# Optimization experiments

Measured on AMD Instinct MI355X. Metric: run time of the kernel, lower is better.

Reference implementation:

```python
import jax, jax.numpy as jnp
import numpy as np

EMB = 768
HEADS = 12
DK = EMB // HEADS
DFF = 3072
LN_EPS = 1e-5


def _layernorm(x, g, b):
    mu = jnp.mean(x, axis=-1, keepdims=True)
    var = jnp.mean(jnp.square(x - mu), axis=-1, keepdims=True)
    return (x - mu) * jax.lax.rsqrt(var + LN_EPS) * g + b


def setup_inputs() -> dict:
    key = jax.random.key(0)
    ks = jax.random.split(key, 16)
    B, S = 16, 577
    s = 0.02
    inp = {
        "x": jax.random.normal(ks[0], (B, S, EMB), jnp.float32),
        # attention projections, stored as [in, out] so y = x @ W + b
        "wq": jax.random.normal(ks[1], (EMB, EMB), jnp.float32) * s,
        "bq": jnp.zeros((EMB,), jnp.float32),
        "wk": jax.random.normal(ks[2], (EMB, EMB), jnp.float32) * s,
        "bk": jnp.zeros((EMB,), jnp.float32),
        "wv": jax.random.normal(ks[3], (EMB, EMB), jnp.float32) * s,
        "bv": jnp.zeros((EMB,), jnp.float32),
        "wo": jax.random.normal(ks[4], (EMB, EMB), jnp.float32) * s,
        "bo": jnp.zeros((EMB,), jnp.float32),
        # feed-forward
        "w1": jax.random.normal(ks[5], (EMB, DFF), jnp.float32) * s,
        "bf1": jnp.zeros((DFF,), jnp.float32),
        "w2": jax.random.normal(ks[6], (DFF, EMB), jnp.float32) * s,
        "bf2": jnp.zeros((EMB,), jnp.float32),
        # layer norms
        "ln1_g": jnp.ones((EMB,), jnp.float32),
        "ln1_b": jnp.zeros((EMB,), jnp.float32),
        "ln2_g": jnp.ones((EMB,), jnp.float32),
        "ln2_b": jnp.zeros((EMB,), jnp.float32),
    }
    return inp


def reference(x, wq, bq, wk, bk, wv, bv, wo, bo, w1, bf1, w2, bf2,
              ln1_g, ln1_b, ln2_g, ln2_b):
    B, S, _ = x.shape
    # --- pre-LN + multi-head attention ---
    residual = x
    h = _layernorm(x, ln1_g, ln1_b)
    q = (h @ wq + bq).reshape(B, S, HEADS, DK)
    k = (h @ wk + bk).reshape(B, S, HEADS, DK)
    v = (h @ wv + bv).reshape(B, S, HEADS, DK)
    # NOTE: source applies softmax to UNSCALED scores (no 1/sqrt(d_k)).
    scores = jnp.einsum("bqhd,bkhd->bhqk", q, k)
    attn = jax.nn.softmax(scores.astype(jnp.float32), axis=-1)
    ctx = jnp.einsum("bhqk,bkhd->bqhd", attn, v).reshape(B, S, EMB)
    h = ctx @ wo + bo
    x = h + residual  # dropout is identity (eval / drop_rate=0)
    # --- pre-LN + feed-forward ---
    residual = x
    h = _layernorm(x, ln2_g, ln2_b)
    h = jax.nn.gelu(h @ w1 + bf1, approximate=False)
    h = h @ w2 + bf2
    return h + residual
```

## Files before the change

kernel.cpp:

```cpp
#include <hip/hip_runtime.h>
#include <hip/hip_bf16.h>
#include <math.h>

#define EMB 768
#define HEADS 12
#define DKH 64
#define DFF 3072
#define NB 16
#define SEQ 577
#define MTOK (NB*SEQ)
#define BHN (NB*HEADS)
#define VLD 640

typedef __attribute__((ext_vector_type(8))) short short8;
typedef __attribute__((ext_vector_type(4))) float f32x4;

__device__ __forceinline__ unsigned short f2bf(float f) {
  __hip_bfloat16 h = __float2bfloat16(f);
  return *reinterpret_cast<unsigned short*>(&h);
}

__device__ __forceinline__ float gelu_f(float x) {
  float u = x * (1.5957691216f + 0.0713548162726f * x * x);
  return x / (1.0f + __expf(-u));
}

__device__ __forceinline__ void gld_lds16(const unsigned short* g, unsigned short* l) {
  __builtin_amdgcn_global_load_lds(
      (const __attribute__((address_space(1))) unsigned int*)(g),
      (__attribute__((address_space(3))) unsigned int*)(l), 16, 0, 0);
}

template<int N> __device__ __forceinline__ void waitcnt_vm() {
  if constexpr (N == 0) asm volatile("s_waitcnt vmcnt(0)" ::: "memory");
  else if constexpr (N == 1) asm volatile("s_waitcnt vmcnt(1)" ::: "memory");
  else if constexpr (N == 2) asm volatile("s_waitcnt vmcnt(2)" ::: "memory");
  else if constexpr (N == 3) asm volatile("s_waitcnt vmcnt(3)" ::: "memory");
  else if constexpr (N == 4) asm volatile("s_waitcnt vmcnt(4)" ::: "memory");
}

__global__ __launch_bounds__(256) void ln_kernel(
    const float* __restrict__ x, const float* __restrict__ g,
    const float* __restrict__ b, unsigned short* __restrict__ out) {
  int row = blockIdx.x;
  int tid = threadIdx.x;
  const float* xr = x + (long)row * EMB;
  float v0 = xr[tid], v1 = xr[tid + 256], v2 = xr[tid + 512];
  float s = v0 + v1 + v2;
  float sq = v0*v0 + v1*v1 + v2*v2;
  for (int off = 32; off; off >>= 1) {
    s  += __shfl_down(s,  off, 64);
    sq += __shfl_down(sq, off, 64);
  }
  __shared__ float sh[8];
  int wid = tid >> 6, lane = tid & 63;
  if (lane == 0) { sh[wid] = s; sh[4 + wid] = sq; }
  __syncthreads();
  s  = sh[0] + sh[1] + sh[2] + sh[3];
  sq = sh[4] + sh[5] + sh[6] + sh[7];
  float mu = s * (1.0f / EMB);
  float var = sq * (1.0f / EMB) - mu * mu;
  float rs = rsqrtf(var + 1e-5f);
  unsigned short* orow = out + (long)row * EMB;
  orow[tid]       = f2bf((v0 - mu) * rs * g[tid]       + b[tid]);
  orow[tid + 256] = f2bf((v1 - mu) * rs * g[tid + 256] + b[tid + 256]);
  orow[tid + 512] = f2bf((v2 - mu) * rs * g[tid + 512] + b[tid + 512]);
}

__global__ __launch_bounds__(256) void transpose_all(
    const float* __restrict__ wq, const float* __restrict__ wk,
    const float* __restrict__ wv, const float* __restrict__ wo,
    const float* __restrict__ w1, const float* __restrict__ w2,
    unsigned short* __restrict__ WqkvT, unsigned short* __restrict__ WoT,
    unsigned short* __restrict__ W1T, unsigned short* __restrict__ W2T) {
  __shared__ float t[32][33];
  const int z = blockIdx.z;
  const int bx = blockIdx.x, by = blockIdx.y;
  const float* src; unsigned short* dst; int R, C, r0, c0;
  if (z < 4) {
    if (bx >= 24) return;
    R = 768; C = 768; r0 = by*32; c0 = bx*32;
    src = (z == 0) ? wq : (z == 1) ? wk : (z == 2) ? wv : wo;
    dst = (z == 0) ? WqkvT : (z == 1) ? WqkvT + 768*768 : (z == 2) ? WqkvT + 2*768*768 : WoT;
  } else if (z == 4) {
    R = 768; C = 3072; r0 = by*32; c0 = bx*32; src = w1; dst = W1T;
  } else {
    R = 3072; C = 768; r0 = bx*32; c0 = by*32; src = w2; dst = W2T;
  }
  int tx = threadIdx.x & 31, ty = threadIdx.x >> 5;
#pragma unroll
  for (int l = 0; l < 4; l++)
    t[ty + l*8][tx] = src[(long)(r0 + ty + l*8) * C + c0 + tx];
  __syncthreads();
#pragma unroll
  for (int l = 0; l < 4; l++)
    dst[(long)(c0 + ty + l*8) * R + r0 + tx] = f2bf(t[tx][ty + l*8]);
}

__global__ void concat_bias(const float* __restrict__ a, const float* __restrict__ b,
                            const float* __restrict__ c, float* __restrict__ o) {
  int i = blockIdx.x * 256 + threadIdx.x;
  if (i < 768) o[i] = a[i];
  else if (i < 1536) o[i] = b[i - 768];
  else if (i < 2304) o[i] = c[i - 1536];
}

__global__ __launch_bounds__(256) void transpose_v(
    const unsigned short* __restrict__ qkv, unsigned short* __restrict__ vT) {
  __shared__ unsigned short t[32][33];
  int bhi = blockIdx.z;
  int b = bhi / HEADS, h = bhi % HEADS;
  int s0 = blockIdx.x * 32, d0 = blockIdx.y * 32;
  int tx = threadIdx.x & 31, ty = threadIdx.x >> 5;
  const unsigned short* base = qkv + ((long)b * SEQ) * (3*EMB) + 2*EMB + h*DKH;
#pragma unroll
  for (int l = 0; l < 4; l++) {
    int s = s0 + ty + l*8;
    t[ty + l*8][tx] = (s < SEQ) ? base[(long)s * (3*EMB) + d0 + tx] : (unsigned short)0;
  }
  __syncthreads();
  unsigned short* ob = vT + ((long)bhi * DKH) * VLD;
#pragma unroll
  for (int l = 0; l < 4; l++) {
    int d = d0 + ty + l*8;
    int s = s0 + tx;
    if (s < SEQ) ob[(long)d * VLD + s] = t[tx][ty + l*8];
  }
}

template<bool BIAS, bool RESID, bool GELU_, bool OF32, int BM, int BN>
__global__ __launch_bounds__(256) void gemm_pipe(
    const unsigned short* __restrict__ A,
    const unsigned short* __restrict__ Bt,
    const float* __restrict__ bias,
    const float* __restrict__ resid,
    float* __restrict__ outf,
    unsigned short* __restrict__ outb,
    int M, int N, int K, int lda, int ldb, int ldc,
    int CX, int CY) {
  constexpr int MT = BM / 32, NT = BN / 32;
  constexpr int MA = BM / 64, NA = BN / 64;
  constexpr int L = MA + NA;
  __shared__ unsigned short As[2][BM * 32];
  __shared__ unsigned short Bs[2][BN * 32];

  const int bid = blockIdx.x;
  const int xcd = bid & 7;
  const int sidx = bid >> 3;
  const int colt = sidx % CX;
  const int band = (sidx / CX) * 8 + xcd;
  if (band >= CY) return;
  const int m0 = band * BM, n0 = colt * BN;

  const int tid = threadIdx.x;
  const int wave = tid >> 6, lane = tid & 63;
  const int wm = (wave >> 1) * (BM / 2), wn = (wave & 1) * (BN / 2);
  const int lm = lane & 15, q = lane >> 4;
  const int qs = ((q ^ ((lm >> 1) & 3)) * 8);

  const int srow = tid >> 2;
  const int scol = (((tid & 3) ^ ((tid >> 3) & 3)) * 8);
  int gmA[MA];
#pragma unroll
  for (int t = 0; t < MA; t++) {
    gmA[t] = m0 + srow + t * 64;
    if (gmA[t] > M - 1) gmA[t] = M - 1;
  }
  int gnB[NA];
#pragma unroll
  for (int t = 0; t < NA; t++) gnB[t] = n0 + srow + t * 64;

  auto stage = [&](int kIter, int buf) {
    const int k0 = kIter << 5;
#pragma unroll
    for (int t = 0; t < MA; t++)
      gld_lds16(A + (long)gmA[t] * lda + k0 + scol, &As[buf][8*tid + t*2048]);
#pragma unroll
    for (int t = 0; t < NA; t++)
      gld_lds16(Bt + (long)gnB[t] * ldb + k0 + scol, &Bs[buf][8*tid + t*2048]);
  };

  f32x4 acc[MT][NT];
#pragma unroll
  for (int i = 0; i < MT; i++)
#pragma unroll
    for (int j = 0; j < NT; j++) acc[i][j] = (f32x4){0,0,0,0};

  const int iters = K >> 5;
  stage(0, 0);
  for (int k = 0; k < iters; k++) {
    const int cur = k & 1;
    if (k + 1 < iters) {
      stage(k + 1, cur ^ 1);
      waitcnt_vm<L>();
    } else {
      waitcnt_vm<0>();
    }
    asm volatile("s_barrier" ::: "memory");

    short8 af[MT], bf[NT];
#pragma unroll
    for (int i = 0; i < MT; i++) af[i] = *(const short8*)&As[cur][(wm + i*16 + lm) * 32 + qs];
#pragma unroll
    for (int j = 0; j < NT; j++) bf[j] = *(const short8*)&Bs[cur][(wn + j*16 + lm) * 32 + qs];
#pragma unroll
    for (int i = 0; i < MT; i++)
#pragma unroll
      for (int j = 0; j < NT; j++)
        acc[i][j] = __builtin_amdgcn_mfma_f32_16x16x32_bf16(af[i], bf[j], acc[i][j], 0, 0, 0);

    asm volatile("s_waitcnt lgkmcnt(0)" ::: "memory");
    asm volatile("s_barrier" ::: "memory");
  }

#pragma unroll
  for (int i = 0; i < MT; i++) {
#pragma unroll
    for (int j = 0; j < NT; j++) {
      int col = n0 + wn + j*16 + lm;
      float bv = BIAS ? bias[col] : 0.0f;
#pragma unroll
      for (int r = 0; r < 4; r++) {
        int row = m0 + wm + i*16 + q*4 + r;
        if (row >= M) continue;
        float v = acc[i][j][r] + bv;
        if (RESID) v += resid[(long)row * ldc + col];
        if (GELU_) v = gelu_f(v);
        long o = (long)row * ldc + col;
        if (OF32)   outf[o] = v;
        else        outb[o] = f2bf(v);
      }
    }
  }
}

#define QT 128
__global__ __launch_bounds__(256) void flash_attn2(
    const unsigned short* __restrict__ qkv,
    const unsigned short* __restrict__ vT,
    unsigned short* __restrict__ ctx) {
  __shared__ unsigned short Qs[QT * 64];
  __shared__ unsigned short Ks[64 * 64];
  __shared__ unsigned short Vs[64 * 64];
  __shared__ unsigned short Ps[QT * 64];

  const int q0 = blockIdx.x * QT;
  const int bh = blockIdx.y;
  const int b = bh / HEADS, h = bh % HEADS;
  const int tid = threadIdx.x;
  const int wave = tid >> 6, lane = tid & 63;
  const int lm = lane & 15, q = lane >> 4;
  const int xlm = (lm >> 1) & 3;

  const int sr = tid >> 3;
  const int gcol = ((tid & 7) ^ ((sr >> 1) & 3)) * 8;

#pragma unroll
  for (int it = 0; it < 4; it++) {
    int r = sr + it*32;
    int s = q0 + r; if (s > SEQ - 1) s = SEQ - 1;
    gld_lds16(qkv + ((long)(b*SEQ + s))*(3*EMB) + h*DKH + gcol, &Qs[8*tid + it*2048]);
  }
  waitcnt_vm<0>();
  __syncthreads();

  short8 qf[2][2];
#pragma unroll
  for (int rt = 0; rt < 2; rt++)
#pragma unroll
    for (int kk = 0; kk < 2; kk++)
      qf[rt][kk] = *(const short8*)&Qs[(wave*32 + rt*16 + lm)*64 + ((kk*4 + q) ^ xlm)*8];

  f32x4 oacc[2][4];
  float lsum[2][4];
#pragma unroll
  for (int rt = 0; rt < 2; rt++)
#pragma unroll
    for (int j = 0; j < 4; j++) oacc[rt][j] = (f32x4){0,0,0,0};
#pragma unroll
  for (int rt = 0; rt < 2; rt++)
#pragma unroll
    for (int r = 0; r < 4; r++) lsum[rt][r] = 0.f;

  for (int kt = 0; kt < 10; kt++) {
    __syncthreads();
#pragma unroll
    for (int it = 0; it < 2; it++) {
      int r = sr + it*32;
      int s = kt*64 + r; if (s > SEQ - 1) s = SEQ - 1;
      gld_lds16(qkv + ((long)(b*SEQ + s))*(3*EMB) + EMB + h*DKH + gcol, &Ks[8*tid + it*2048]);
      gld_lds16(vT + ((long)bh*DKH + r)*VLD + (long)kt*64 + gcol, &Vs[8*tid + it*2048]);
    }
    waitcnt_vm<0>();
    __syncthreads();

    f32x4 sacc[2][4];
#pragma unroll
    for (int t = 0; t < 4; t++) {
      short8 kf0 = *(const short8*)&Ks[(t*16 + lm)*64 + ((0 + q) ^ xlm)*8];
      short8 kf1 = *(const short8*)&Ks[(t*16 + lm)*64 + ((4 + q) ^ xlm)*8];
      bool dead = (kt*64 + t*16 + lm) >= SEQ;
#pragma unroll
      for (int rt = 0; rt < 2; rt++) {
        f32x4 s0 = __builtin_amdgcn_mfma_f32_16x16x32_bf16(qf[rt][0], kf0, (f32x4){0,0,0,0}, 0, 0, 0);
        s0 = __builtin_amdgcn_mfma_f32_16x16x32_bf16(qf[rt][1], kf1, s0, 0, 0, 0);
        sacc[rt][t] = dead ? (f32x4){-1e30f,-1e30f,-1e30f,-1e30f} : s0;
      }
    }

#pragma unroll
    for (int rt = 0; rt < 2; rt++)
#pragma unroll
      for (int t = 0; t < 4; t++)
#pragma unroll
        for (int r = 0; r < 4; r++) {
          float p = __expf(sacc[rt][t][r] - 8.0f);
          lsum[rt][r] += p;
          int row = wave*32 + rt*16 + q*4 + r;
          int g = (t*2 + (lm >> 3)) ^ ((q*2 + (r >> 1)) & 3);
          Ps[row*64 + g*8 + (lm & 7)] = f2bf(p);
        }

#pragma unroll
    for (int kk = 0; kk < 2; kk++) {
      short8 vf[4];
#pragma unroll
      for (int j = 0; j < 4; j++)
        vf[j] = *(const short8*)&Vs[(j*16 + lm)*64 + ((kk*4 + q) ^ xlm)*8];
#pragma unroll
      for (int rt = 0; rt < 2; rt++) {
        short8 pf = *(const short8*)&Ps[(wave*32 + rt*16 + lm)*64 + ((kk*4 + q) ^ xlm)*8];
#pragma unroll
        for (int j = 0; j < 4; j++)
          oacc[rt][j] = __builtin_amdgcn_mfma_f32_16x16x32_bf16(pf, vf[j], oacc[rt][j], 0, 0, 0);
      }
    }
  }

#pragma unroll
  for (int rt = 0; rt < 2; rt++)
#pragma unroll
    for (int r = 0; r < 4; r++) {
      float l = lsum[rt][r];
      l += __shfl_xor(l, 1, 64);
      l += __shfl_xor(l, 2, 64);
      l += __shfl_xor(l, 4, 64);
      l += __shfl_xor(l, 8, 64);
      lsum[rt][r] = 1.0f / l;
    }

#pragma unroll
  for (int rt = 0; rt < 2; rt++)
#pragma unroll
    for (int j = 0; j < 4; j++)
#pragma unroll
      for (int r = 0; r < 4; r++) {
        int row = q0 + wave*32 + rt*16 + q*4 + r;
        if (row < SEQ)
          ctx[((long)(b*SEQ + row))*EMB + h*DKH + j*16 + lm] =
              f2bf(oacc[rt][j][r] * lsum[rt][r]);
      }
}

extern "C" void kernel_launch(void* const* d_in, const int* in_sizes, int n_in,
                              void* d_out, int out_size, void* d_ws, size_t ws_size,
                              hipStream_t stream) {
  const float* x     = (const float*)d_in[0];
  const float* wq    = (const float*)d_in[1];
  const float* bq    = (const float*)d_in[2];
  const float* wk    = (const float*)d_in[3];
  const float* bk    = (const float*)d_in[4];
  const float* wv    = (const float*)d_in[5];
  const float* bv    = (const float*)d_in[6];
  const float* wo    = (const float*)d_in[7];
  const float* bo    = (const float*)d_in[8];
  const float* w1    = (const float*)d_in[9];
  const float* bf1   = (const float*)d_in[10];
  const float* w2    = (const float*)d_in[11];
  const float* bf2   = (const float*)d_in[12];
  const float* ln1g  = (const float*)d_in[13];
  const float* ln1b  = (const float*)d_in[14];
  const float* ln2g  = (const float*)d_in[15];
  const float* ln2b  = (const float*)d_in[16];
  float* out = (float*)d_out;

  char* w = (char*)d_ws;
  size_t off = 0;
  auto alloc = [&](size_t bytes) -> void* {
    void* p = w + off;
    off = (off + bytes + 255) & ~(size_t)255;
    return p;
  };
  unsigned short* WqkvT = (unsigned short*)alloc((size_t)3 * 768 * 768 * 2);
  unsigned short* WoT   = (unsigned short*)alloc((size_t)768 * 768 * 2);
  unsigned short* W1T   = (unsigned short*)alloc((size_t)3072 * 768 * 2);
  unsigned short* W2T   = (unsigned short*)alloc((size_t)768 * 3072 * 2);
  float*          bqkv  = (float*)alloc(2304 * 4);
  unsigned short* hbuf  = (unsigned short*)alloc((size_t)MTOK * EMB * 2);
  unsigned short* qkv   = (unsigned short*)alloc((size_t)MTOK * 3 * EMB * 2);
  unsigned short* vT    = (unsigned short*)alloc((size_t)BHN * DKH * VLD * 2);
  float*          x1    = (float*)alloc((size_t)MTOK * EMB * 4);
  unsigned short* g     = (unsigned short*)alloc((size_t)MTOK * DFF * 2);
  (void)ws_size; (void)in_sizes; (void)n_in; (void)out_size;

  dim3 blk(256);
  const int B128 = ((73 + 7) / 8) * 8;

  transpose_all<<<dim3(96, 24, 6), blk, 0, stream>>>(
      wq, wk, wv, wo, w1, w2, WqkvT, WoT, W1T, W2T);
  concat_bias<<<dim3(9), blk, 0, stream>>>(bq, bk, bv, bqkv);

  ln_kernel<<<dim3(MTOK), blk, 0, stream>>>(x, ln1g, ln1b, hbuf);

  gemm_pipe<true, false, false, false, 128, 128><<<dim3(18 * B128), blk, 0, stream>>>(
      hbuf, WqkvT, bqkv, nullptr, nullptr, qkv,
      MTOK, 3*EMB, EMB, EMB, EMB, 3*EMB, 18, 73);

  transpose_v<<<dim3(19, 2, BHN), blk, 0, stream>>>(qkv, vT);

  flash_attn2<<<dim3(5, BHN), blk, 0, stream>>>(qkv, vT, hbuf);

  gemm_pipe<true, true, false, true, 128, 64><<<dim3(12 * B128), blk, 0, stream>>>(
      hbuf, WoT, bo, x, x1, nullptr,
      MTOK, EMB, EMB, EMB, EMB, EMB, 12, 73);

  ln_kernel<<<dim3(MTOK), blk, 0, stream>>>(x1, ln2g, ln2b, hbuf);

  gemm_pipe<true, false, true, false, 128, 128><<<dim3(24 * B128), blk, 0, stream>>>(
      hbuf, W1T, bf1, nullptr, nullptr, g,
      MTOK, DFF, EMB, EMB, EMB, DFF, 24, 73);

  gemm_pipe<true, true, false, true, 128, 64><<<dim3(12 * B128), blk, 0, stream>>>(
      g, W2T, bf2, x1, out, nullptr,
      MTOK, EMB, DFF, DFF, DFF, EMB, 12, 73);
}
```

Baseline: 471.7 us.

## Triple-buffer GEMM LDS pipeline, serpentine tile order, fold bias concat into transpose

The GEMM main loop goes from double to triple buffering, prefetching two K-steps ahead with a matching vmcnt wait, so global-to-LDS loads have more time to overlap MFMA work. Column tile order is reversed on alternate band groups, a serpentine walk meant to improve L2 reuse of B tiles between neighbouring block groups. The separate bias-concatenation kernel is folded into the weight transpose launch as an extra z-slice, which removes one launch. The trade-off is 50% more LDS per block, which may lower occupancy.

Measured after the change: 475.0 us. Within noise of the previous version (+0.7%).

```diff
diff --git a/kernel.cpp b/kernel.cpp
--- a/kernel.cpp
+++ b/kernel.cpp
@@ -37,6 +37,9 @@
   else if constexpr (N == 2) asm volatile("s_waitcnt vmcnt(2)" ::: "memory");
   else if constexpr (N == 3) asm volatile("s_waitcnt vmcnt(3)" ::: "memory");
   else if constexpr (N == 4) asm volatile("s_waitcnt vmcnt(4)" ::: "memory");
+  else if constexpr (N == 5) asm volatile("s_waitcnt vmcnt(5)" ::: "memory");
+  else if constexpr (N == 6) asm volatile("s_waitcnt vmcnt(6)" ::: "memory");
+  else if constexpr (N == 8) asm volatile("s_waitcnt vmcnt(8)" ::: "memory");
 }
 
 __global__ __launch_bounds__(256) void ln_kernel(
@@ -71,11 +74,23 @@
     const float* __restrict__ wq, const float* __restrict__ wk,
     const float* __restrict__ wv, const float* __restrict__ wo,
     const float* __restrict__ w1, const float* __restrict__ w2,
+    const float* __restrict__ bq, const float* __restrict__ bk,
+    const float* __restrict__ bv,
     unsigned short* __restrict__ WqkvT, unsigned short* __restrict__ WoT,
-    unsigned short* __restrict__ W1T, unsigned short* __restrict__ W2T) {
+    unsigned short* __restrict__ W1T, unsigned short* __restrict__ W2T,
+    float* __restrict__ bqkv) {
   __shared__ float t[32][33];
   const int z = blockIdx.z;
   const int bx = blockIdx.x, by = blockIdx.y;
+  if (z == 6) {
+    if (by == 0 && bx < 9) {
+      int i = bx * 256 + threadIdx.x;
+      if (i < 768) bqkv[i] = bq[i];
+      else if (i < 1536) bqkv[i] = bk[i - 768];
+      else if (i < 2304) bqkv[i] = bv[i - 1536];
+    }
+    return;
+  }
   const float* src; unsigned short* dst; int R, C, r0, c0;
   if (z < 4) {
     if (bx >= 24) return;
@@ -95,14 +110,6 @@
 #pragma unroll
   for (int l = 0; l < 4; l++)
     dst[(long)(c0 + ty + l*8) * R + r0 + tx] = f2bf(t[tx][ty + l*8]);
-}
-
-__global__ void concat_bias(const float* __restrict__ a, const float* __restrict__ b,
-                            const float* __restrict__ c, float* __restrict__ o) {
-  int i = blockIdx.x * 256 + threadIdx.x;
-  if (i < 768) o[i] = a[i];
-  else if (i < 1536) o[i] = b[i - 768];
-  else if (i < 2304) o[i] = c[i - 1536];
 }
 
 __global__ __launch_bounds__(256) void transpose_v(
@@ -141,14 +148,16 @@
   constexpr int MT = BM / 32, NT = BN / 32;
   constexpr int MA = BM / 64, NA = BN / 64;
   constexpr int L = MA + NA;
-  __shared__ unsigned short As[2][BM * 32];
-  __shared__ unsigned short Bs[2][BN * 32];
+  __shared__ unsigned short As[3][BM * 32];
+  __shared__ unsigned short Bs[3][BN * 32];
 
   const int bid = blockIdx.x;
   const int xcd = bid & 7;
   const int sidx = bid >> 3;
-  const int colt = sidx % CX;
-  const int band = (sidx / CX) * 8 + xcd;
+  const int bg = sidx / CX;
+  int colt = sidx % CX;
+  if (bg & 1) colt = CX - 1 - colt;
+  const int band = bg * 8 + xcd;
   if (band >= CY) return;
   const int m0 = band * BM, n0 = colt * BN;
 
@@ -188,10 +197,14 @@
 
   const int iters = K >> 5;
   stage(0, 0);
+  stage(1, 1);
+  int cur = 0;
   for (int k = 0; k < iters; k++) {
-    const int cur = k & 1;
-    if (k + 1 < iters) {
-      stage(k + 1, cur ^ 1);
+    if (k + 2 < iters) {
+      int nb = cur + 2; if (nb >= 3) nb -= 3;
+      stage(k + 2, nb);
+      waitcnt_vm<2 * L>();
+    } else if (k + 1 < iters) {
       waitcnt_vm<L>();
     } else {
       waitcnt_vm<0>();
@@ -211,6 +224,7 @@
 
     asm volatile("s_waitcnt lgkmcnt(0)" ::: "memory");
     asm volatile("s_barrier" ::: "memory");
+    cur++; if (cur >= 3) cur = 0;
   }
 
 #pragma unroll
@@ -406,9 +420,8 @@
   dim3 blk(256);
   const int B128 = ((73 + 7) / 8) * 8;
 
-  transpose_all<<<dim3(96, 24, 6), blk, 0, stream>>>(
-      wq, wk, wv, wo, w1, w2, WqkvT, WoT, W1T, W2T);
-  concat_bias<<<dim3(9), blk, 0, stream>>>(bq, bk, bv, bqkv);
+  transpose_all<<<dim3(96, 24, 7), blk, 0, stream>>>(
+      wq, wk, wv, wo, w1, w2, bq, bk, bv, WqkvT, WoT, W1T, W2T, bqkv);
 
   ln_kernel<<<dim3(MTOK), blk, 0, stream>>>(x, ln1g, ln1b, hbuf);
 
```
